# Optimization experiments

Hardware: AMD Instinct MI355X
Metric: run time of the kernel (lower is better)

## Reference

```python
import jax, jax.numpy as jnp
import numpy as np

# Dims: M=batch, T=time frames, B=bottleneck channels, H=intermediate channels, KK=kernel size
M, T, B, H, KK = 8, 4000, 128, 512, 3
DILATION = 2
EPS = 1e-8  # gLN eps (ConvTasNet convention)


def prelu(x, a):
    return jnp.where(x >= 0, x, a * x)


def gln(x, gamma, beta):
    # global layer norm over (time, channel) per sample; x: [M, T, C]
    m = jnp.mean(x, axis=(1, 2), keepdims=True)
    v = jnp.mean((x - m) ** 2, axis=(1, 2), keepdims=True)
    return gamma * (x - m) / jnp.sqrt(v + EPS) + beta


def depthwise_conv_same_reflect(x, w):
    # x: [M, C, L], w: [C, K]; dilation 1, 'same' padding with reflect mode
    K = w.shape[1]
    pl = (K - 1) // 2
    xp = jnp.pad(x, ((0, 0), (0, 0), (pl, K - 1 - pl)), mode='reflect')
    return jax.lax.conv_general_dilated(
        xp, w[:, None, :], (1,), 'VALID',
        feature_group_count=x.shape[1], dimension_numbers=('NCH', 'OIH', 'NCH'))


def setup_inputs() -> dict:
    key = jax.random.key(0)
    ks = jax.random.split(key, 12)
    f32 = jnp.float32
    return {
        'x': jax.random.normal(ks[0], (M, T, B), f32),
        'conv1_w': jax.random.normal(ks[1], (H, B), f32) * 0.05,
        'prelu1_a': jnp.asarray(0.25, f32),
        'norm1_g': jnp.ones((H,), f32),
        'norm1_b': jnp.zeros((H,), f32),
        'off_dw_w': jax.random.normal(ks[2], (H, KK), f32) * 0.02,
        'odc_prelu_a': jnp.asarray(0.25, f32),
        'off_pw_w': jax.random.normal(ks[3], (KK, H), f32) * 0.02,
        'opc_prelu_a': jnp.asarray(0.25, f32),
        'dw_w': jax.random.normal(ks[4], (H, KK), f32) * 0.05,
        'dw_b': jax.random.normal(ks[5], (H,), f32) * 0.01,
        'prelu2_a': jnp.asarray(0.25, f32),
        'norm2_g': jnp.ones((H,), f32),
        'norm2_b': jnp.zeros((H,), f32),
        'pw_w': jax.random.normal(ks[6], (B, H), f32) * 0.05,
    }


def reference(x, conv1_w, prelu1_a, norm1_g, norm1_b,
              off_dw_w, odc_prelu_a, off_pw_w, opc_prelu_a,
              dw_w, dw_b, prelu2_a, norm2_g, norm2_b, pw_w):
    dtype = x.dtype
    residual = x
    # 1x1 bottleneck conv -> PReLU -> gLN
    h = jnp.einsum('mtb,hb->mth', x, conv1_w)
    h = gln(prelu(h, prelu1_a), norm1_g, norm1_b)
    hc = jnp.moveaxis(h, 1, 2)  # [M, H, T]

    # --- offset prediction branch (PackedDeformConv1d) ---
    off = depthwise_conv_same_reflect(hc, off_dw_w)          # [M, H, T]
    off = prelu(off, odc_prelu_a)
    off = jnp.einsum('mct,kc->mkt', off, off_pw_w)           # [M, KK, T]
    off = prelu(off, opc_prelu_a)
    offsets = jnp.moveaxis(off, 1, 2)                        # [M, T, KK]

    # --- deformable depthwise conv (same padding, reflect) ---
    pad_tot = DILATION * (KK - 1)
    pl = pad_tot // 2
    xp = jnp.pad(hc, ((0, 0), (0, 0), (pl, pad_tot - pl)), mode='reflect')  # [M,H,Lp]
    Lp = T + pad_tot
    dil_pos = (jnp.arange(KK) * DILATION).astype(dtype)      # [KK]: 0, d, 2d
    t0 = jnp.arange(T, dtype=dtype)[:, None]                 # [T,1]
    Tpos = t0 + dil_pos[None, :] + offsets                   # [M,T,KK]
    Tpos = jnp.clip(Tpos, t0, t0 + dil_pos[-1])              # constrain to receptive field
    U = jnp.clip(jnp.floor(Tpos).astype(jnp.int32), 0, Lp - 2)
    Uf = U.astype(dtype)
    g0 = jax.nn.relu(1.0 - jnp.abs(Uf - Tpos))               # [M,T,KK]
    g1 = jax.nn.relu(1.0 - jnp.abs(Uf + 1.0 - Tpos))
    idx = jnp.broadcast_to(U.reshape(M, 1, T * KK), (M, H, T * KK))
    s0 = jnp.take_along_axis(xp, idx, axis=2).reshape(M, H, T, KK)
    s1 = jnp.take_along_axis(xp, idx + 1, axis=2).reshape(M, H, T, KK)
    sampled = g0[:, None] * s0 + g1[:, None] * s1            # [M,H,T,KK]
    y = jnp.einsum('mhtk,hk->mht', sampled, dw_w) + dw_b[None, :, None]

    # PReLU -> gLN -> 1x1 conv back to B channels, residual add
    y = jnp.moveaxis(y, 1, 2)                                # [M,T,H]
    y = gln(prelu(y, prelu2_a), norm2_g, norm2_b)
    out = jnp.einsum('mth,bh->mtb', y, pw_w)
    return out + residual
```

## Files before the change

kernel.cpp:

```cpp
#include <hip/hip_runtime.h>

#define Mdim 8
#define Tdim 4000
#define Bdim 128
#define Hdim 512
#define NPER (Tdim*Hdim)
#define EPSG 1e-8f

typedef __attribute__((ext_vector_type(8))) short short8;
typedef __attribute__((ext_vector_type(4))) float floatx4;

static __device__ __forceinline__ float bits2f(unsigned short s) {
  union { unsigned int u; float f; } v; v.u = ((unsigned int)s) << 16; return v.f;
}
static __device__ __forceinline__ unsigned short f2bits(float f) {
  union { float f; unsigned int u; } v; v.f = f;
  unsigned int u = v.u;
  u += 0x7fffu + ((u >> 16) & 1u);
  return (unsigned short)(u >> 16);
}
static __device__ __forceinline__ short8 pack8(const float4& a, const float4& b) {
  short8 v;
  v[0]=(short)f2bits(a.x); v[1]=(short)f2bits(a.y); v[2]=(short)f2bits(a.z); v[3]=(short)f2bits(a.w);
  v[4]=(short)f2bits(b.x); v[5]=(short)f2bits(b.y); v[6]=(short)f2bits(b.z); v[7]=(short)f2bits(b.w);
  return v;
}

#define LDS_FENCE() do { \
  asm volatile("s_waitcnt lgkmcnt(0)" ::: "memory"); \
  __builtin_amdgcn_sched_barrier(0); \
} while (0)


__global__ __launch_bounds__(256) void k_prep(
    const float* __restrict__ w1,
    const float* __restrict__ pww,
    const float* __restrict__ g2w,
    const float* __restrict__ b2w,
    unsigned short* __restrict__ w1r,
    unsigned short* __restrict__ W2g,
    float* __restrict__ Sv,
    float* __restrict__ B2s)
{
  const int tid = threadIdx.x;
  if (blockIdx.x < 32) {
    int i = blockIdx.x*256 + tid;
    int lane = i & 63, f = i >> 6;
    int nt = f & 3, ks = (f >> 2) & 3, hc = f >> 4;
    int h = hc*64 + nt*16 + (lane & 15);
    int c = ks*32 + (lane >> 4)*8;
    const float* src = &w1[(size_t)h*Bdim + c];
    float4 a = *(const float4*)src;
    float4 b = *(const float4*)(src + 4);
    *(short8*)&w1r[(size_t)i*8] = pack8(a, b);
  } else {
    const int b = (blockIdx.x - 32)*4 + (tid >> 6);
    const int sub = tid & 63;
    const int j8 = sub*8;
    float pv[8], g2v[8], b2v[8];
    #pragma unroll
    for (int j = 0; j < 8; j += 4) {
      *(float4*)&pv[j]  = *(const float4*)&pww[(size_t)b*Hdim + j8 + j];
      *(float4*)&g2v[j] = *(const float4*)&g2w[j8 + j];
      *(float4*)&b2v[j] = *(const float4*)&b2w[j8 + j];
    }
    float sS = 0.f, sB = 0.f;
    short8 wv8;
    #pragma unroll
    for (int j = 0; j < 8; ++j) {
      float pg = pv[j]*g2v[j];
      sS += pg;
      sB += pv[j]*b2v[j];
      wv8[j] = (short)f2bits(pg);
    }
    {
      int half = b >> 6, nt = (b >> 4) & 3, l16 = b & 15;
      int kc = sub >> 4, ks = (sub >> 2) & 3, quad = sub & 3;
      int lane = quad*16 + l16;
      size_t f = (((size_t)(half*4 + kc)*4 + ks)*4 + nt);
      *(short8*)&W2g[(f*64 + lane)*8] = wv8;
    }
    #pragma unroll
    for (int st = 32; st > 0; st >>= 1) { sS += __shfl_xor(sS, st); sB += __shfl_xor(sB, st); }
    if (sub == 0) { Sv[b] = sS; B2s[b] = sB; }
  }
}

__global__ __launch_bounds__(256) void k_conv1(
    const float* __restrict__ x,
    const unsigned short* __restrict__ w1r,
    const float* __restrict__ a1p,
    unsigned short* __restrict__ Hbuf,
    float2* __restrict__ part1)
{
  __shared__ __align__(16) unsigned short ltile[4][16*72];
  __shared__ float red[512];

  const int tid = threadIdx.x;
  const int n = blockIdx.x + 125*blockIdx.y;
  const int m  = n & 7;
  const int tile = n >> 3;
  const int t0 = tile * 32;
  const int lane = tid & 63, w = tid >> 6, quad = lane >> 4, l16 = lane & 15;
  const int tsub = w & 1, hh = w >> 1;
  const int tbase = t0 + tsub*16;
  const float* xrow = x + ((size_t)m*Tdim + tbase + l16)*Bdim;
  short8 afr[4];
  #pragma unroll
  for (int ks = 0; ks < 4; ++ks) {
    float4 fa = *(const float4*)&xrow[ks*32 + quad*8];
    float4 fb = *(const float4*)&xrow[ks*32 + quad*8 + 4];
    afr[ks] = pack8(fa, fb);
  }

  const float a1 = a1p[0];
  const short8* wf = (const short8*)w1r + lane;
  float lsum = 0.f, lss = 0.f;

  #pragma unroll
  for (int hc4 = 0; hc4 < 4; ++hc4) {
    const int hcg = hh*4 + hc4;
    floatx4 acc[4] = {};
    #pragma unroll
    for (int ks = 0; ks < 4; ++ks)
      #pragma unroll
      for (int nt = 0; nt < 4; ++nt)
        acc[nt] = __builtin_amdgcn_mfma_f32_16x16x32_bf16(
            afr[ks], wf[(hcg*16 + ks*4 + nt)*64], acc[nt], 0, 0, 0);

    #pragma unroll
    for (int nt = 0; nt < 4; ++nt) {
      int hl = nt*16 + l16;
      #pragma unroll
      for (int r = 0; r < 4; ++r) {
        int tl = quad*4 + r;
        float v = acc[nt][r];
        v = v >= 0.f ? v : a1 * v;
        lsum += v; lss += v*v;
        ltile[w][tl*72 + hl] = f2bits(v);
      }
    }
    LDS_FENCE();
    {
      int row = lane >> 2, ck = (lane & 3) * 16;
      unsigned short* dst = &Hbuf[((size_t)m*Tdim + tbase + row)*Hdim + hcg*64 + ck];
      *(short8*)&dst[0] = *(const short8*)&ltile[w][row*72 + ck];
      *(short8*)&dst[8] = *(const short8*)&ltile[w][row*72 + ck + 8];
    }
    LDS_FENCE();
  }

  red[tid] = lsum; red[256 + tid] = lss;
  __syncthreads();
  for (int s = 128; s > 0; s >>= 1) {
    if (tid < s) { red[tid] += red[tid + s]; red[256+tid] += red[256+tid+s]; }
    __syncthreads();
  }
  if (tid == 0)
    part1[(size_t)m*125 + tile] = make_float2(red[0], red[256]);
}

__global__ __launch_bounds__(256) void k_deform(
    const unsigned short* __restrict__ Hbuf,
    const float2* __restrict__ part1,
    const float* __restrict__ g1w,
    const float* __restrict__ b1w,
    const float* __restrict__ odw,
    const float* __restrict__ aodcp,
    const float* __restrict__ opw,
    const float* __restrict__ aopcp,
    const float* __restrict__ dww,
    const float* __restrict__ dwb,
    const float* __restrict__ a2p,
    unsigned short* __restrict__ Ybuf,
    float2* __restrict__ part2)
{
  __shared__ float s_stats[2];
  __shared__ float rsum[4], rss[4];
  const int tid = threadIdx.x, lane = tid & 63, w = tid >> 6;
  const int n = blockIdx.x + 500*blockIdx.y;
  const int m  = n & 7;
  const int tx = n >> 3;
  const int tb = tx*8 + w*2;
  const int c8 = lane*8;
  const unsigned short* base = Hbuf + (size_t)m*Tdim*Hdim;

  short8 hrow[2][3];
  #pragma unroll
  for (int tt = 0; tt < 2; ++tt) {
    int t = tb + tt;
    int tm1 = (t == 0) ? 1 : t-1;
    int tp1 = (t == Tdim-1) ? Tdim-2 : t+1;
    hrow[tt][0] = *(const short8*)&base[(size_t)tm1*Hdim + c8];
    hrow[tt][1] = *(const short8*)&base[(size_t)t  *Hdim + c8];
    hrow[tt][2] = *(const short8*)&base[(size_t)tp1*Hdim + c8];
  }
  float g1v[8], b1v[8];
  #pragma unroll
  for (int j = 0; j < 8; j += 4) {
    *(float4*)&g1v[j] = *(const float4*)&g1w[c8 + j];
    *(float4*)&b1v[j] = *(const float4*)&b1w[c8 + j];
  }

  if (tid < 64) {
    float s = 0.f, q = 0.f;
    for (int i = lane; i < 125; i += 64) {
      float2 p = part1[(size_t)m*125 + i];
      s += p.x; q += p.y;
    }
    #pragma unroll
    for (int st = 32; st > 0; st >>= 1) { s += __shfl_xor(s, st); q += __shfl_xor(q, st); }
    if (lane == 0) { s_stats[0] = s; s_stats[1] = q; }
  }
  __syncthreads();
  const float invn = 1.0f/(float)NPER;
  const float mean1 = s_stats[0]*invn;
  const float var1  = fmaxf(s_stats[1]*invn - mean1*mean1, 0.f);
  const float inv1  = 1.0f/sqrtf(var1 + EPSG);

  float oa[2][3] = {};
  {
    const float aodc = aodcp[0];
    float wod[24], q0v[8], q1v[8], q2v[8];
    #pragma unroll
    for (int j = 0; j < 8; j += 4) {
      *(float4*)&q0v[j] = *(const float4*)&opw[c8 + j];
      *(float4*)&q1v[j] = *(const float4*)&opw[Hdim + c8 + j];
      *(float4*)&q2v[j] = *(const float4*)&opw[2*Hdim + c8 + j];
    }
    #pragma unroll
    for (int j = 0; j < 24; j += 4)
      *(float4*)&wod[j] = *(const float4*)&odw[c8*3 + j];

    #pragma unroll
    for (int j = 0; j < 8; ++j) {
      float A = g1v[j] * inv1;
      float C = b1v[j] - mean1*A;
      #pragma unroll
      for (int tt = 0; tt < 2; ++tt) {
        float fm = fmaf(A, bits2f((unsigned short)hrow[tt][0][j]), C);
        float fz = fmaf(A, bits2f((unsigned short)hrow[tt][1][j]), C);
        float fp = fmaf(A, bits2f((unsigned short)hrow[tt][2][j]), C);
        float d = fm*wod[j*3+0] + fz*wod[j*3+1] + fp*wod[j*3+2];
        d = d >= 0.f ? d : aodc*d;
        oa[tt][0] = fmaf(d, q0v[j], oa[tt][0]);
        oa[tt][1] = fmaf(d, q1v[j], oa[tt][1]);
        oa[tt][2] = fmaf(d, q2v[j], oa[tt][2]);
      }
    }
    #pragma unroll
    for (int s = 32; s > 0; s >>= 1) {
      #pragma unroll
      for (int tt = 0; tt < 2; ++tt) {
        oa[tt][0] += __shfl_xor(oa[tt][0], s);
        oa[tt][1] += __shfl_xor(oa[tt][1], s);
        oa[tt][2] += __shfl_xor(oa[tt][2], s);
      }
    }
  }

  const float aopc = aopcp[0];
  const float a2   = a2p[0];
  int I0[2][3], I1[2][3]; float G0[2][3], G1[2][3], GS[2][3];
  #pragma unroll
  for (int tt = 0; tt < 2; ++tt) {
    const float tf = (float)(tb + tt);
    #pragma unroll
    for (int k = 0; k < 3; ++k) {
      float off = oa[tt][k];
      off = off >= 0.f ? off : aopc*off;
      float pos = tf + (float)(2*k) + off;
      pos = fminf(fmaxf(pos, tf), tf + 4.0f);
      int U = (int)floorf(pos);
      if (U > Tdim + 2) U = Tdim + 2;
      float Uf = (float)U;
      G0[tt][k] = fmaxf(0.f, 1.f - fabsf(Uf - pos));
      G1[tt][k] = fmaxf(0.f, 1.f - fabsf(Uf + 1.f - pos));
      GS[tt][k] = G0[tt][k] + G1[tt][k];
      int ia = U - 2; ia = ia < 0 ? -ia : ia; if (ia > Tdim-1) ia = 2*(Tdim-1) - ia;
      int ib = U - 1; ib = ib < 0 ? -ib : ib; if (ib > Tdim-1) ib = 2*(Tdim-1) - ib;
      I0[tt][k] = ia; I1[tt][k] = ib;
    }
  }

  short8 s0v[2][3], s1v[2][3];
  #pragma unroll
  for (int tt = 0; tt < 2; ++tt)
    #pragma unroll
    for (int k = 0; k < 3; ++k) {
      s0v[tt][k] = *(const short8*)&base[(size_t)I0[tt][k]*Hdim + c8];
      s1v[tt][k] = *(const short8*)&base[(size_t)I1[tt][k]*Hdim + c8];
    }

  float bv[8], wd[24];
  #pragma unroll
  for (int j = 0; j < 8; j += 4)
    *(float4*)&bv[j] = *(const float4*)&dwb[c8 + j];
  #pragma unroll
  for (int j = 0; j < 24; j += 4)
    *(float4*)&wd[j] = *(const float4*)&dww[c8*3 + j];

  float lsum = 0.f, lss = 0.f;
  short8 yv[2];
  #pragma unroll
  for (int j = 0; j < 8; ++j) {
    float A = g1v[j] * inv1;
    float C = b1v[j] - mean1*A;
    float w0 = wd[j*3+0], w1 = wd[j*3+1], w2 = wd[j*3+2];
    #pragma unroll
    for (int tt = 0; tt < 2; ++tt) {
      float ybase = fmaf(C, w0*GS[tt][0] + w1*GS[tt][1] + w2*GS[tt][2], bv[j]);
      float t0s = fmaf(G1[tt][0], bits2f((unsigned short)s1v[tt][0][j]), G0[tt][0]*bits2f((unsigned short)s0v[tt][0][j]));
      float t1s = fmaf(G1[tt][1], bits2f((unsigned short)s1v[tt][1][j]), G0[tt][1]*bits2f((unsigned short)s0v[tt][1][j]));
      float t2s = fmaf(G1[tt][2], bits2f((unsigned short)s1v[tt][2][j]), G0[tt][2]*bits2f((unsigned short)s0v[tt][2][j]));
      float acc = w0*t0s + w1*t1s + w2*t2s;
      float y = fmaf(A, acc, ybase);
      float p = y >= 0.f ? y : a2*y;
      lsum += p; lss += p*p;
      yv[tt][j] = (short)f2bits(p);
    }
  }
  #pragma unroll
  for (int tt = 0; tt < 2; ++tt)
    *(short8*)&Ybuf[((size_t)m*Tdim + tb + tt)*Hdim + c8] = yv[tt];

  #pragma unroll
  for (int s = 32; s > 0; s >>= 1) {
    lsum += __shfl_xor(lsum, s);
    lss  += __shfl_xor(lss, s);
  }
  if (lane == 0) { rsum[w] = lsum; rss[w] = lss; }
  __syncthreads();
  if (tid == 0)
    part2[(size_t)m*500 + tx] =
      make_float2(rsum[0]+rsum[1]+rsum[2]+rsum[3], rss[0]+rss[1]+rss[2]+rss[3]);
}

__global__ __launch_bounds__(256) void k_out(
    const unsigned short* __restrict__ Ybuf,
    const unsigned short* __restrict__ W2g,
    const float2* __restrict__ part2,
    const float* __restrict__ Sv,
    const float* __restrict__ B2s,
    const float* __restrict__ x,
    float* __restrict__ out)
{
  __shared__ __align__(16) float ltf[64*68];
  __shared__ float rsA[4], rsB[4];
  const int tid = threadIdx.x;
  const int n = blockIdx.x + 63*(blockIdx.y + 2*blockIdx.z);
  const int m = n & 7;
  const int r = n >> 3;
  const int tile = r >> 1, half = r & 1;
  const int t0 = tile*64;
  const int n0 = half*64;
  const int lane = tid & 63, wv = tid >> 6, quad = lane >> 4, l16 = lane & 15;

  {
    float s = 0.f, q = 0.f;
    for (int i = tid; i < 500; i += 256) {
      float2 p = part2[(size_t)m*500 + i];
      s += p.x; q += p.y;
    }
    #pragma unroll
    for (int st = 32; st > 0; st >>= 1) { s += __shfl_xor(s, st); q += __shfl_xor(q, st); }
    if (lane == 0) { rsA[wv] = s; rsB[wv] = q; }
  }

  int tr = t0 + wv*16 + l16;
  int trc = tr < Tdim ? tr : Tdim-1;
  const unsigned short* arow = Ybuf + ((size_t)m*Tdim + trc)*Hdim;
  const short8* wf = (const short8*)W2g + (size_t)half*64*64 + lane;

  floatx4 acc[4] = {};
  #pragma unroll
  for (int kc = 0; kc < 4; ++kc)
    #pragma unroll
    for (int ks = 0; ks < 4; ++ks) {
      short8 afr = *(const short8*)&arow[kc*128 + ks*32 + quad*8];
      #pragma unroll
      for (int nt = 0; nt < 4; ++nt)
        acc[nt] = __builtin_amdgcn_mfma_f32_16x16x32_bf16(
            afr, wf[((kc*4 + ks)*4 + nt)*64], acc[nt], 0, 0, 0);
    }

  __syncthreads();
  const float Ssum = rsA[0]+rsA[1]+rsA[2]+rsA[3];
  const float Qsum = rsB[0]+rsB[1]+rsB[2]+rsB[3];
  const float invn = 1.0f/(float)NPER;
  const float mean2 = Ssum*invn;
  const float var2  = fmaxf(Qsum*invn - mean2*mean2, 0.f);
  const float inv2  = 1.0f/sqrtf(var2 + EPSG);
  const float ms2   = inv2*mean2;

  #pragma unroll
  for (int nt = 0; nt < 4; ++nt) {
    int bl = nt*16 + l16;
    float cb = B2s[n0 + bl] - ms2*Sv[n0 + bl];
    #pragma unroll
    for (int r2 = 0; r2 < 4; ++r2) {
      int tl = wv*16 + quad*4 + r2;
      ltf[tl*68 + bl] = fmaf(inv2, acc[nt][r2], cb);
    }
  }
  LDS_FENCE();
  {
    int tr2 = tid >> 2, ck = (tid & 3) * 16;
    int tg = t0 + tr2;
    if (tg < Tdim) {
      const float* xr = &x[((size_t)m*Tdim + tg)*Bdim + n0 + ck];
      float* orow = &out[((size_t)m*Tdim + tg)*Bdim + n0 + ck];
      #pragma unroll
      for (int j = 0; j < 4; ++j) {
        float4 v = *(const float4*)&ltf[tr2*68 + ck + j*4];
        float4 rx = *(const float4*)&xr[j*4];
        v.x += rx.x; v.y += rx.y; v.z += rx.z; v.w += rx.w;
        *(float4*)&orow[j*4] = v;
      }
    }
  }
}

extern "C" void kernel_launch(void* const* d_in, const int* in_sizes, int n_in,
                              void* d_out, int out_size, void* d_ws, size_t ws_size,
                              hipStream_t stream)
{
  (void)in_sizes; (void)n_in; (void)out_size; (void)ws_size;
  const float* x    = (const float*)d_in[0];
  const float* w1   = (const float*)d_in[1];
  const float* a1   = (const float*)d_in[2];
  const float* g1   = (const float*)d_in[3];
  const float* b1   = (const float*)d_in[4];
  const float* odw  = (const float*)d_in[5];
  const float* aodc = (const float*)d_in[6];
  const float* opw  = (const float*)d_in[7];
  const float* aopc = (const float*)d_in[8];
  const float* dww  = (const float*)d_in[9];
  const float* dwb  = (const float*)d_in[10];
  const float* a2   = (const float*)d_in[11];
  const float* g2   = (const float*)d_in[12];
  const float* b2   = (const float*)d_in[13];
  const float* pww  = (const float*)d_in[14];
  float* out = (float*)d_out;

  char* ws = (char*)d_ws;
  const size_t OFF_P1  = 0;
  const size_t OFF_P2  = 8192;
  const size_t OFF_S   = 40960;
  const size_t OFF_B2S = 41472;
  const size_t OFF_W1R = 45056;
  const size_t OFF_W2G = 176128;
  const size_t OFF_H   = 307200;
  const size_t OFF_Y   = 33075200;
  float2* part1 = (float2*)(ws + OFF_P1);
  float2* part2 = (float2*)(ws + OFF_P2);
  float*  Sv    = (float*)(ws + OFF_S);
  float*  B2s   = (float*)(ws + OFF_B2S);
  unsigned short* w1r  = (unsigned short*)(ws + OFF_W1R);
  unsigned short* W2g  = (unsigned short*)(ws + OFF_W2G);
  unsigned short* Hbuf = (unsigned short*)(ws + OFF_H);
  unsigned short* Ybuf = (unsigned short*)(ws + OFF_Y);

  k_prep  <<<dim3(64), 256, 0, stream>>>(w1, pww, g2, b2, w1r, W2g, Sv, B2s);
  k_conv1 <<<dim3(125, 8), 256, 0, stream>>>(x, w1r, a1, Hbuf, part1);
  k_deform<<<dim3(500, 8), 256, 0, stream>>>(Hbuf, part1, g1, b1, odw, aodc, opw, aopc, dww, dwb, a2, Ybuf, part2);
  k_out   <<<dim3(63, 2, 8), 256, 0, stream>>>(Ybuf, W2g, part2, Sv, B2s, x, out);
}
```

Measured before the change: 165.7 us.

## Fuse deformable conv with output pointwise GEMM via LDS tile, defer gLN2 to epilogue

The deform kernel now processes 32 time steps per block, stages the bf16 PReLU output in shared memory, and runs the 512->128 MFMA GEMM in place. It writes raw fp32 GEMM results (Graw) instead of the bf16 Y intermediate. A light finishing kernel applies the gLN2 affine correction, which is linear and so can be applied after the GEMM, then adds the residual. This removes the Y round-trip through global memory, but the fp32 Graw buffer (M*T*128*4 bytes) is still written and read, and each block now has fewer blocks in flight with a serial 4-iteration loop.

```diff
diff --git a/kernel.cpp b/kernel.cpp
--- a/kernel.cpp
+++ b/kernel.cpp
@@ -6,6 +6,7 @@
 #define Hdim 512
 #define NPER (Tdim*Hdim)
 #define EPSG 1e-8f
+#define YSTR 520
 
 typedef __attribute__((ext_vector_type(8))) short short8;
 typedef __attribute__((ext_vector_type(4))) float floatx4;
@@ -30,7 +31,6 @@
   asm volatile("s_waitcnt lgkmcnt(0)" ::: "memory"); \
   __builtin_amdgcn_sched_barrier(0); \
 } while (0)
-
 
 __global__ __launch_bounds__(256) void k_prep(
     const float* __restrict__ w1,
@@ -160,7 +160,7 @@
     part1[(size_t)m*125 + tile] = make_float2(red[0], red[256]);
 }
 
-__global__ __launch_bounds__(256) void k_deform(
+__global__ __launch_bounds__(256) void k_dfg(
     const unsigned short* __restrict__ Hbuf,
     const float2* __restrict__ part1,
     const float* __restrict__ g1w,
@@ -172,35 +172,21 @@
     const float* __restrict__ dww,
     const float* __restrict__ dwb,
     const float* __restrict__ a2p,
-    unsigned short* __restrict__ Ybuf,
+    const unsigned short* __restrict__ W2g,
+    float* __restrict__ Graw,
     float2* __restrict__ part2)
 {
+  __shared__ __align__(16) unsigned short ytile[32*YSTR];
   __shared__ float s_stats[2];
-  __shared__ float rsum[4], rss[4];
+  __shared__ float rsA[4], rsB[4];
   const int tid = threadIdx.x, lane = tid & 63, w = tid >> 6;
-  const int n = blockIdx.x + 500*blockIdx.y;
-  const int m  = n & 7;
-  const int tx = n >> 3;
-  const int tb = tx*8 + w*2;
+  const int quad = lane >> 4, l16 = lane & 15;
+  const int n = blockIdx.x + 125*blockIdx.y;
+  const int m    = n & 7;
+  const int tile = n >> 3;
+  const int t0   = tile * 32;
   const int c8 = lane*8;
   const unsigned short* base = Hbuf + (size_t)m*Tdim*Hdim;
-
-  short8 hrow[2][3];
-  #pragma unroll
-  for (int tt = 0; tt < 2; ++tt) {
-    int t = tb + tt;
-    int tm1 = (t == 0) ? 1 : t-1;
-    int tp1 = (t == Tdim-1) ? Tdim-2 : t+1;
-    hrow[tt][0] = *(const short8*)&base[(size_t)tm1*Hdim + c8];
-    hrow[tt][1] = *(const short8*)&base[(size_t)t  *Hdim + c8];
-    hrow[tt][2] = *(const short8*)&base[(size_t)tp1*Hdim + c8];
-  }
-  float g1v[8], b1v[8];
-  #pragma unroll
-  for (int j = 0; j < 8; j += 4) {
-    *(float4*)&g1v[j] = *(const float4*)&g1w[c8 + j];
-    *(float4*)&b1v[j] = *(const float4*)&b1w[c8 + j];
-  }
 
   if (tid < 64) {
     float s = 0.f, q = 0.f;
@@ -218,20 +204,41 @@
   const float var1  = fmaxf(s_stats[1]*invn - mean1*mean1, 0.f);
   const float inv1  = 1.0f/sqrtf(var1 + EPSG);
 
-  float oa[2][3] = {};
-  {
-    const float aodc = aodcp[0];
-    float wod[24], q0v[8], q1v[8], q2v[8];
-    #pragma unroll
-    for (int j = 0; j < 8; j += 4) {
-      *(float4*)&q0v[j] = *(const float4*)&opw[c8 + j];
-      *(float4*)&q1v[j] = *(const float4*)&opw[Hdim + c8 + j];
-      *(float4*)&q2v[j] = *(const float4*)&opw[2*Hdim + c8 + j];
-    }
-    #pragma unroll
-    for (int j = 0; j < 24; j += 4)
-      *(float4*)&wod[j] = *(const float4*)&odw[c8*3 + j];
-
+  const float aodc = aodcp[0], aopc = aopcp[0], a2 = a2p[0];
+  float g1v[8], b1v[8], wod[24], q0v[8], q1v[8], q2v[8], wd[24], bv[8];
+  #pragma unroll
+  for (int j = 0; j < 8; j += 4) {
+    *(float4*)&g1v[j] = *(const float4*)&g1w[c8 + j];
+    *(float4*)&b1v[j] = *(const float4*)&b1w[c8 + j];
+    *(float4*)&q0v[j] = *(const float4*)&opw[c8 + j];
+    *(float4*)&q1v[j] = *(const float4*)&opw[Hdim + c8 + j];
+    *(float4*)&q2v[j] = *(const float4*)&opw[2*Hdim + c8 + j];
+    *(float4*)&bv[j]  = *(const float4*)&dwb[c8 + j];
+  }
+  #pragma unroll
+  for (int j = 0; j < 24; j += 4) {
+    *(float4*)&wod[j] = *(const float4*)&odw[c8*3 + j];
+    *(float4*)&wd[j]  = *(const float4*)&dww[c8*3 + j];
+  }
+
+  float lsum = 0.f, lss = 0.f;
+
+  #pragma unroll 1
+  for (int it = 0; it < 4; ++it) {
+    const int tb = t0 + w*8 + it*2;
+
+    short8 hrow[2][3];
+    #pragma unroll
+    for (int tt = 0; tt < 2; ++tt) {
+      int t = tb + tt;
+      int tm1 = (t == 0) ? 1 : t-1;
+      int tp1 = (t == Tdim-1) ? Tdim-2 : t+1;
+      hrow[tt][0] = *(const short8*)&base[(size_t)tm1*Hdim + c8];
+      hrow[tt][1] = *(const short8*)&base[(size_t)t  *Hdim + c8];
+      hrow[tt][2] = *(const short8*)&base[(size_t)tp1*Hdim + c8];
+    }
+
+    float oa[2][3] = {};
     #pragma unroll
     for (int j = 0; j < 8; ++j) {
       float A = g1v[j] * inv1;
@@ -257,133 +264,127 @@
         oa[tt][2] += __shfl_xor(oa[tt][2], s);
       }
     }
-  }
-
-  const float aopc = aopcp[0];
-  const float a2   = a2p[0];
-  int I0[2][3], I1[2][3]; float G0[2][3], G1[2][3], GS[2][3];
-  #pragma unroll
-  for (int tt = 0; tt < 2; ++tt) {
-    const float tf = (float)(tb + tt);
-    #pragma unroll
-    for (int k = 0; k < 3; ++k) {
-      float off = oa[tt][k];
-      off = off >= 0.f ? off : aopc*off;
-      float pos = tf + (float)(2*k) + off;
-      pos = fminf(fmaxf(pos, tf), tf + 4.0f);
-      int U = (int)floorf(pos);
-      if (U > Tdim + 2) U = Tdim + 2;
-      float Uf = (float)U;
-      G0[tt][k] = fmaxf(0.f, 1.f - fabsf(Uf - pos));
-      G1[tt][k] = fmaxf(0.f, 1.f - fabsf(Uf + 1.f - pos));
-      GS[tt][k] = G0[tt][k] + G1[tt][k];
-      int ia = U - 2; ia = ia < 0 ? -ia : ia; if (ia > Tdim-1) ia = 2*(Tdim-1) - ia;
-      int ib = U - 1; ib = ib < 0 ? -ib : ib; if (ib > Tdim-1) ib = 2*(Tdim-1) - ib;
-      I0[tt][k] = ia; I1[tt][k] = ib;
-    }
-  }
-
-  short8 s0v[2][3], s1v[2][3];
-  #pragma unroll
-  for (int tt = 0; tt < 2; ++tt)
-    #pragma unroll
-    for (int k = 0; k < 3; ++k) {
-      s0v[tt][k] = *(const short8*)&base[(size_t)I0[tt][k]*Hdim + c8];
-      s1v[tt][k] = *(const short8*)&base[(size_t)I1[tt][k]*Hdim + c8];
-    }
-
-  float bv[8], wd[24];
-  #pragma unroll
-  for (int j = 0; j < 8; j += 4)
-    *(float4*)&bv[j] = *(const float4*)&dwb[c8 + j];
-  #pragma unroll
-  for (int j = 0; j < 24; j += 4)
-    *(float4*)&wd[j] = *(const float4*)&dww[c8*3 + j];
-
-  float lsum = 0.f, lss = 0.f;
-  short8 yv[2];
-  #pragma unroll
-  for (int j = 0; j < 8; ++j) {
-    float A = g1v[j] * inv1;
-    float C = b1v[j] - mean1*A;
-    float w0 = wd[j*3+0], w1 = wd[j*3+1], w2 = wd[j*3+2];
+
+    int I0[2][3], I1[2][3]; float G0[2][3], G1[2][3], GS[2][3];
     #pragma unroll
     for (int tt = 0; tt < 2; ++tt) {
-      float ybase = fmaf(C, w0*GS[tt][0] + w1*GS[tt][1] + w2*GS[tt][2], bv[j]);
-      float t0s = fmaf(G1[tt][0], bits2f((unsigned short)s1v[tt][0][j]), G0[tt][0]*bits2f((unsigned short)s0v[tt][0][j]));
-      float t1s = fmaf(G1[tt][1], bits2f((unsigned short)s1v[tt][1][j]), G0[tt][1]*bits2f((unsigned short)s0v[tt][1][j]));
-      float t2s = fmaf(G1[tt][2], bits2f((unsigned short)s1v[tt][2][j]), G0[tt][2]*bits2f((unsigned short)s0v[tt][2][j]));
-      float acc = w0*t0s + w1*t1s + w2*t2s;
-      float y = fmaf(A, acc, ybase);
-      float p = y >= 0.f ? y : a2*y;
-      lsum += p; lss += p*p;
-      yv[tt][j] = (short)f2bits(p);
-    }
-  }
-  #pragma unroll
-  for (int tt = 0; tt < 2; ++tt)
-    *(short8*)&Ybuf[((size_t)m*Tdim + tb + tt)*Hdim + c8] = yv[tt];
+      const float tf = (float)(tb + tt);
+      #pragma unroll
+      for (int k = 0; k < 3; ++k) {
+        float off = oa[tt][k];
+        off = off >= 0.f ? off : aopc*off;
+        float pos = tf + (float)(2*k) + off;
+        pos = fminf(fmaxf(pos, tf), tf + 4.0f);
+        int U = (int)floorf(pos);
+        if (U > Tdim + 2) U = Tdim + 2;
+        float Uf = (float)U;
+        G0[tt][k] = fmaxf(0.f, 1.f - fabsf(Uf - pos));
+        G1[tt][k] = fmaxf(0.f, 1.f - fabsf(Uf + 1.f - pos));
+        GS[tt][k] = G0[tt][k] + G1[tt][k];
+        int ia = U - 2; ia = ia < 0 ? -ia : ia; if (ia > Tdim-1) ia = 2*(Tdim-1) - ia;
+        int ib = U - 1; ib = ib < 0 ? -ib : ib; if (ib > Tdim-1) ib = 2*(Tdim-1) - ib;
+        I0[tt][k] = ia; I1[tt][k] = ib;
+      }
+    }
+
+    short8 s0v[2][3], s1v[2][3];
+    #pragma unroll
+    for (int tt = 0; tt < 2; ++tt)
+      #pragma unroll
+      for (int k = 0; k < 3; ++k) {
+        s0v[tt][k] = *(const short8*)&base[(size_t)I0[tt][k]*Hdim + c8];
+        s1v[tt][k] = *(const short8*)&base[(size_t)I1[tt][k]*Hdim + c8];
+      }
+
+    short8 yv[2];
+    #pragma unroll
+    for (int j = 0; j < 8; ++j) {
+      float A = g1v[j] * inv1;
+      float C = b1v[j] - mean1*A;
+      float w0 = wd[j*3+0], w1 = wd[j*3+1], w2 = wd[j*3+2];
+      #pragma unroll
+      for (int tt = 0; tt < 2; ++tt) {
+        float ybase = fmaf(C, w0*GS[tt][0] + w1*GS[tt][1] + w2*GS[tt][2], bv[j]);
+        float t0s = fmaf(G1[tt][0], bits2f((unsigned short)s1v[tt][0][j]), G0[tt][0]*bits2f((unsigned short)s0v[tt][0][j]));
+        float t1s = fmaf(G1[tt][1], bits2f((unsigned short)s1v[tt][1][j]), G0[tt][1]*bits2f((unsigned short)s0v[tt][1][j]));
+        float t2s = fmaf(G1[tt][2], bits2f((unsigned short)s1v[tt][2][j]), G0[tt][2]*bits2f((unsigned short)s0v[tt][2][j]));
+        float acc = w0*t0s + w1*t1s + w2*t2s;
+        float y = fmaf(A, acc, ybase);
+        float p = y >= 0.f ? y : a2*y;
+        lsum += p; lss += p*p;
+        yv[tt][j] = (short)f2bits(p);
+      }
+    }
+    #pragma unroll
+    for (int tt = 0; tt < 2; ++tt)
+      *(short8*)&ytile[(w*8 + it*2 + tt)*YSTR + c8] = yv[tt];
+  }
+
+  __syncthreads();
+
+  {
+    const int stripe = (w & 1) * 16;
+    const int half   = w >> 1;
+    const short8* wf = (const short8*)W2g + (size_t)half*64*64 + lane;
+    floatx4 acc[4] = {};
+    #pragma unroll
+    for (int kc = 0; kc < 4; ++kc)
+      #pragma unroll
+      for (int ks = 0; ks < 4; ++ks) {
+        short8 afr = *(const short8*)&ytile[(stripe + l16)*YSTR + kc*128 + ks*32 + quad*8];
+        #pragma unroll
+        for (int nt = 0; nt < 4; ++nt)
+          acc[nt] = __builtin_amdgcn_mfma_f32_16x16x32_bf16(
+              afr, wf[((kc*4 + ks)*4 + nt)*64], acc[nt], 0, 0, 0);
+      }
+    #pragma unroll
+    for (int nt = 0; nt < 4; ++nt) {
+      int col = half*64 + nt*16 + l16;
+      #pragma unroll
+      for (int r = 0; r < 4; ++r) {
+        int row = stripe + quad*4 + r;
+        Graw[((size_t)m*Tdim + t0 + row)*Bdim + col] = acc[nt][r];
+      }
+    }
+  }
 
   #pragma unroll
   for (int s = 32; s > 0; s >>= 1) {
     lsum += __shfl_xor(lsum, s);
     lss  += __shfl_xor(lss, s);
   }
-  if (lane == 0) { rsum[w] = lsum; rss[w] = lss; }
+  if (lane == 0) { rsA[w] = lsum; rsB[w] = lss; }
   __syncthreads();
   if (tid == 0)
-    part2[(size_t)m*500 + tx] =
-      make_float2(rsum[0]+rsum[1]+rsum[2]+rsum[3], rss[0]+rss[1]+rss[2]+rss[3]);
-}
-
-__global__ __launch_bounds__(256) void k_out(
-    const unsigned short* __restrict__ Ybuf,
-    const unsigned short* __restrict__ W2g,
+    part2[(size_t)m*125 + tile] =
+      make_float2(rsA[0]+rsA[1]+rsA[2]+rsA[3], rsB[0]+rsB[1]+rsB[2]+rsB[3]);
+}
+
+__global__ __launch_bounds__(256) void k_fin(
+    const float* __restrict__ Graw,
     const float2* __restrict__ part2,
     const float* __restrict__ Sv,
     const float* __restrict__ B2s,
     const float* __restrict__ x,
     float* __restrict__ out)
 {
-  __shared__ __align__(16) float ltf[64*68];
   __shared__ float rsA[4], rsB[4];
-  const int tid = threadIdx.x;
-  const int n = blockIdx.x + 63*(blockIdx.y + 2*blockIdx.z);
-  const int m = n & 7;
-  const int r = n >> 3;
-  const int tile = r >> 1, half = r & 1;
-  const int t0 = tile*64;
-  const int n0 = half*64;
-  const int lane = tid & 63, wv = tid >> 6, quad = lane >> 4, l16 = lane & 15;
+  const int tid = threadIdx.x, lane = tid & 63, wv = tid >> 6;
+  const int n = blockIdx.x + 125*blockIdx.y;
+  const int m    = n & 7;
+  const int tile = n >> 3;
+  const int t0   = tile * 32;
 
   {
     float s = 0.f, q = 0.f;
-    for (int i = tid; i < 500; i += 256) {
-      float2 p = part2[(size_t)m*500 + i];
+    for (int i = tid; i < 125; i += 256) {
+      float2 p = part2[(size_t)m*125 + i];
       s += p.x; q += p.y;
     }
     #pragma unroll
     for (int st = 32; st > 0; st >>= 1) { s += __shfl_xor(s, st); q += __shfl_xor(q, st); }
     if (lane == 0) { rsA[wv] = s; rsB[wv] = q; }
   }
-
-  int tr = t0 + wv*16 + l16;
-  int trc = tr < Tdim ? tr : Tdim-1;
-  const unsigned short* arow = Ybuf + ((size_t)m*Tdim + trc)*Hdim;
-  const short8* wf = (const short8*)W2g + (size_t)half*64*64 + lane;
-
-  floatx4 acc[4] = {};
-  #pragma unroll
-  for (int kc = 0; kc < 4; ++kc)
-    #pragma unroll
-    for (int ks = 0; ks < 4; ++ks) {
-      short8 afr = *(const short8*)&arow[kc*128 + ks*32 + quad*8];
-      #pragma unroll
-      for (int nt = 0; nt < 4; ++nt)
-        acc[nt] = __builtin_amdgcn_mfma_f32_16x16x32_bf16(
-            afr, wf[((kc*4 + ks)*4 + nt)*64], acc[nt], 0, 0, 0);
-    }
-
   __syncthreads();
   const float Ssum = rsA[0]+rsA[1]+rsA[2]+rsA[3];
   const float Qsum = rsB[0]+rsB[1]+rsB[2]+rsB[3];
@@ -393,31 +394,24 @@
   const float inv2  = 1.0f/sqrtf(var2 + EPSG);
   const float ms2   = inv2*mean2;
 
-  #pragma unroll
-  for (int nt = 0; nt < 4; ++nt) {
-    int bl = nt*16 + l16;
-    float cb = B2s[n0 + bl] - ms2*Sv[n0 + bl];
-    #pragma unroll
-    for (int r2 = 0; r2 < 4; ++r2) {
-      int tl = wv*16 + quad*4 + r2;
-      ltf[tl*68 + bl] = fmaf(inv2, acc[nt][r2], cb);
-    }
-  }
-  LDS_FENCE();
-  {
-    int tr2 = tid >> 2, ck = (tid & 3) * 16;
-    int tg = t0 + tr2;
-    if (tg < Tdim) {
-      const float* xr = &x[((size_t)m*Tdim + tg)*Bdim + n0 + ck];
-      float* orow = &out[((size_t)m*Tdim + tg)*Bdim + n0 + ck];
-      #pragma unroll
-      for (int j = 0; j < 4; ++j) {
-        float4 v = *(const float4*)&ltf[tr2*68 + ck + j*4];
-        float4 rx = *(const float4*)&xr[j*4];
-        v.x += rx.x; v.y += rx.y; v.z += rx.z; v.w += rx.w;
-        *(float4*)&orow[j*4] = v;
-      }
-    }
+  const int row = tid >> 3;
+  const int c0  = (tid & 7) * 16;
+  const size_t off = ((size_t)m*Tdim + t0 + row)*Bdim + c0;
+  const float* gr = Graw + off;
+  const float* xr = x + off;
+  float* orow = out + off;
+  #pragma unroll
+  for (int j = 0; j < 4; ++j) {
+    float4 G  = *(const float4*)&gr[j*4];
+    float4 xs = *(const float4*)&xr[j*4];
+    float4 B2 = *(const float4*)&B2s[c0 + j*4];
+    float4 Sq = *(const float4*)&Sv[c0 + j*4];
+    float4 v;
+    v.x = fmaf(inv2, G.x, B2.x - ms2*Sq.x) + xs.x;
+    v.y = fmaf(inv2, G.y, B2.y - ms2*Sq.y) + xs.y;
+    v.z = fmaf(inv2, G.z, B2.z - ms2*Sq.z) + xs.z;
+    v.w = fmaf(inv2, G.w, B2.w - ms2*Sq.w) + xs.w;
+    *(float4*)&orow[j*4] = v;
   }
 }
 
@@ -446,12 +440,12 @@
   char* ws = (char*)d_ws;
   const size_t OFF_P1  = 0;
   const size_t OFF_P2  = 8192;
-  const size_t OFF_S   = 40960;
-  const size_t OFF_B2S = 41472;
-  const size_t OFF_W1R = 45056;
-  const size_t OFF_W2G = 176128;
-  const size_t OFF_H   = 307200;
-  const size_t OFF_Y   = 33075200;
+  const size_t OFF_S   = 16384;
+  const size_t OFF_B2S = 16896;
+  const size_t OFF_W1R = 17408;
+  const size_t OFF_W2G = 148480;
+  const size_t OFF_H   = 279552;
+  const size_t OFF_G   = 33047552;
   float2* part1 = (float2*)(ws + OFF_P1);
   float2* part2 = (float2*)(ws + OFF_P2);
   float*  Sv    = (float*)(ws + OFF_S);
@@ -459,10 +453,10 @@
   unsigned short* w1r  = (unsigned short*)(ws + OFF_W1R);
   unsigned short* W2g  = (unsigned short*)(ws + OFF_W2G);
   unsigned short* Hbuf = (unsigned short*)(ws + OFF_H);
-  unsigned short* Ybuf = (unsigned short*)(ws + OFF_Y);
+  float* Graw = (float*)(ws + OFF_G);
 
   k_prep  <<<dim3(64), 256, 0, stream>>>(w1, pww, g2, b2, w1r, W2g, Sv, B2s);
   k_conv1 <<<dim3(125, 8), 256, 0, stream>>>(x, w1r, a1, Hbuf, part1);
-  k_deform<<<dim3(500, 8), 256, 0, stream>>>(Hbuf, part1, g1, b1, odw, aodc, opw, aopc, dww, dwb, a2, Ybuf, part2);
-  k_out   <<<dim3(63, 2, 8), 256, 0, stream>>>(Ybuf, W2g, part2, Sv, B2s, x, out);
-}
+  k_dfg   <<<dim3(125, 8), 256, 0, stream>>>(Hbuf, part1, g1, b1, odw, aodc, opw, aopc, dww, dwb, a2, W2g, Graw, part2);
+  k_fin   <<<dim3(125, 8), 256, 0, stream>>>(Graw, part2, Sv, B2s, x, out);
+}
```

Result: slower. 182.0 us (+9.9%).
